# Performance work log

Measured on AMD Instinct MI355X. Metric: run time of the kernel, lower is better.

Reference implementation:

```python
import math
import jax, jax.numpy as jnp
import numpy as np

CHUNK = 32
EPS = 1e-5


def l2norm(x):
    return x * jax.lax.rsqrt(jnp.sum(x * x, -1, keepdims=True))


def causal_dwconv(x, w):
    # x: (B, C, L); w: (C, K) depthwise causal conv (left pad K-1)
    C, K = w.shape
    return jax.lax.conv_general_dilated(x, w[:, None, :], (1,), [(K - 1, 0)], feature_group_count=C)


def per_head_stats(x):
    # x: (B,L,H,D) -> (B,L,H,4): mean, var(pop), abs-mean, l2-norm
    mean = jnp.mean(x, -1, keepdims=True)
    var = jnp.mean(x * x, -1, keepdims=True) - mean * mean
    abs_mean = jnp.mean(jnp.abs(x), -1, keepdims=True)
    l2 = jnp.sqrt(jnp.sum(x * x, -1, keepdims=True))
    return jnp.concatenate([mean, var, abs_mean, l2], -1)


def delta_rule_chunkwise(q, k, v, beta, chunk=CHUNK):
    # q,k: (B,H,L,dk); v: (B,H,L,dv); beta: (B,H,L)
    b, h, L, dk = q.shape
    dv = v.shape[-1]
    pad = (-L) % chunk
    if pad:
        pc = ((0, 0), (0, 0), (0, pad), (0, 0))
        q, k, v = (jnp.pad(t, pc) for t in (q, k, v))
        beta = jnp.pad(beta, ((0, 0), (0, 0), (0, pad)))
    Lp = L + pad
    n = Lp // chunk
    q = l2norm(q)
    k = l2norm(k)
    v = v * beta[..., None]
    kb = k * beta[..., None]
    resh = lambda t: t.reshape(b, h, n, chunk, t.shape[-1])
    q, k, v, kb = map(resh, (q, k, v, kb))
    tri = jnp.triu(jnp.ones((chunk, chunk), bool))          # incl. diag
    strict = jnp.triu(jnp.ones((chunk, chunk), bool), 1)    # above diag
    A = jnp.where(tri, 0.0, -jnp.einsum('bhncd,bhned->bhnce', kb, k))
    # forward-substitution inverse of (I - strict_lower) as in the torch loop
    for i in range(1, chunk):
        upd = jnp.einsum('...k,...kj->...j', A[..., i, :], A[..., :, :i])
        A = A.at[..., i, :i].add(upd)
    inv = A + jnp.eye(chunk, dtype=A.dtype)
    u = inv @ v   # (b,h,n,c,dv)
    w = inv @ kb  # (b,h,n,c,dk)

    def step(S, xs):
        qi, ki, ui, wi = xs  # (b,h,c,d)
        attn = jnp.where(strict, 0.0, qi @ jnp.swapaxes(ki, -1, -2))
        u_adj = ui - wi @ S
        out_i = qi @ S + attn @ u_adj
        S = S + jnp.swapaxes(ki, -1, -2) @ u_adj
        return S, out_i

    xs = tuple(jnp.moveaxis(t, 2, 0) for t in (q, k, u, w))
    S0 = jnp.zeros((b, h, dk, dv), q.dtype)
    S, outs = jax.lax.scan(step, S0, xs)
    out = jnp.moveaxis(outs, 0, 2).reshape(b, h, Lp, dv)[:, :, :L]
    return out, S


def reference(hidden_states, q_proj_w, k_proj_w, v_proj_w, b_proj_w,
              q_conv_w, k_conv_w, v_conv_w, fir_short_w, fir_long_w,
              fuse_w1, fuse_b1, fuse_w2, fuse_b2, logit_temp,
              res_scale_short, res_scale_long, o_norm_w, o_proj_w):
    B, L, D = hidden_states.shape
    H = fir_short_w.shape[0]

    def shortconv(x, w):  # x: (B,L,C)
        y = causal_dwconv(jnp.swapaxes(x, 1, 2), w)
        return jax.nn.silu(jnp.swapaxes(y, 1, 2))

    q = shortconv(hidden_states @ q_proj_w.T, q_conv_w)
    k = shortconv(hidden_states @ k_proj_w.T, k_conv_w)
    v = shortconv(hidden_states @ v_proj_w.T, v_conv_w)
    q = q.reshape(B, L, H, -1)
    k = k.reshape(B, L, H, -1)
    v_direct = v.reshape(B, L, H, -1)
    beta = jax.nn.sigmoid(hidden_states @ b_proj_w.T)  # (B,L,H)

    delta_out, _S = delta_rule_chunkwise(
        jnp.transpose(q, (0, 2, 1, 3)), jnp.transpose(k, (0, 2, 1, 3)),
        jnp.transpose(v_direct, (0, 2, 1, 3)), jnp.transpose(beta, (0, 2, 1)))
    delta_out = jnp.transpose(delta_out, (0, 2, 1, 3))

    def fir(x, filt):  # x: (B,L,H,Dh); filt: (H,Dh,K)
        hh, dd, kk = filt.shape
        xf = jnp.swapaxes(x.reshape(B, L, hh * dd), 1, 2)
        y = causal_dwconv(xf, filt.reshape(hh * dd, kk))
        return jnp.swapaxes(y, 1, 2).reshape(B, L, hh, dd)

    local_short = fir(v_direct, fir_short_w)
    local_long = fir(v_direct, fir_long_w)

    stats = jnp.concatenate([per_head_stats(t) for t in
                             (local_short, local_long, delta_out, v_direct)], -1)  # (B,L,H,16)
    hs_exp = jnp.broadcast_to(hidden_states[:, :, None, :], (B, L, H, D))
    gate_in = jnp.concatenate([hs_exp, stats], -1)
    hdn = jax.nn.gelu(gate_in @ fuse_w1.T + fuse_b1, approximate=False)
    logits = hdn @ fuse_w2.T + fuse_b2  # (B,L,H,4)
    temp = jax.nn.softplus(logit_temp) + 1e-4
    fw = jax.nn.softmax(logits / temp, -1)

    o = (fw[..., 0:1] * local_short + fw[..., 1:2] * local_long
         + fw[..., 2:3] * delta_out + fw[..., 3:4] * v_direct)
    o = o + res_scale_short * local_short + res_scale_long * local_long
    o = o * jax.lax.rsqrt(jnp.mean(o * o, -1, keepdims=True) + EPS) * o_norm_w
    return o.reshape(B, L, -1) @ o_proj_w.T


def setup_inputs() -> dict:
    key = jax.random.key(0)
    ks = jax.random.split(key, 16)
    B, L, D, H = 2, 4096, 1024, 4
    dk, dv = D, D
    dh = dv // H
    gate_in_dim = D + 16
    gate_hidden = D * 2 // 2
    s = 0.02
    f32 = jnp.float32
    return {
        'hidden_states': jax.random.normal(ks[0], (B, L, D), f32),
        'q_proj_w': jax.random.normal(ks[1], (dk, D), f32) * s,
        'k_proj_w': jax.random.normal(ks[2], (dk, D), f32) * s,
        'v_proj_w': jax.random.normal(ks[3], (dv, D), f32) * s,
        'b_proj_w': jax.random.normal(ks[4], (H, D), f32) * s,
        'q_conv_w': jax.random.normal(ks[5], (dk, 4), f32) * 0.1,
        'k_conv_w': jax.random.normal(ks[6], (dk, 4), f32) * 0.1,
        'v_conv_w': jax.random.normal(ks[7], (dv, 4), f32) * 0.1,
        'fir_short_w': jax.random.normal(ks[8], (H, dh, 5), f32) * 0.02,
        'fir_long_w': jax.random.normal(ks[9], (H, dh, 64), f32) * 0.02,
        'fuse_w1': jax.random.normal(ks[10], (gate_hidden, gate_in_dim), f32) * s,
        'fuse_b1': jnp.zeros((gate_hidden,), f32),
        'fuse_w2': jax.random.normal(ks[11], (4, gate_hidden), f32) * s,
        'fuse_b2': jnp.array([-1.0, -1.0, 1.0, 3.0], f32),
        'logit_temp': jnp.full((1,), math.log(math.expm1(0.7)), f32),
        'res_scale_short': jnp.full((1,), 0.1, f32),
        'res_scale_long': jnp.full((1,), 0.1, f32),
        'o_norm_w': jnp.ones((dh,), f32),
        'o_proj_w': jax.random.normal(ks[12], (D, dv), f32) * s,
    }
```

## Files before the change

### kernel.cpp

```cpp
#include <hip/hip_runtime.h>
#include <hip/hip_bf16.h>

#define BB 2
#define LL 4096
#define DD 1024
#define HH 4
#define DH 256
#define CH 32
#define NC (LL/CH)
#define BL (BB*LL)
#define BLD ((size_t)BB*LL*DD)

typedef __attribute__((ext_vector_type(8))) short short8;
typedef __attribute__((ext_vector_type(4))) float floatx4;

__device__ __forceinline__ float bf2f(unsigned short u) {
    union { float f; unsigned int i; } x; x.i = ((unsigned int)u) << 16; return x.f;
}
__device__ __forceinline__ float bflo(unsigned int u) {
    union { float f; unsigned int i; } x; x.i = u << 16; return x.f;
}
__device__ __forceinline__ float bfhi(unsigned int u) {
    union { float f; unsigned int i; } x; x.i = u & 0xFFFF0000u; return x.f;
}
__device__ __forceinline__ unsigned short f2bf(float f) {
    union { float f; unsigned int i; } x; x.f = f;
    unsigned int r = x.i + 0x7FFFu + ((x.i >> 16) & 1u);
    return (unsigned short)(r >> 16);
}
__device__ __forceinline__ unsigned int pkbf(float a, float b) {
    unsigned int ua = __float_as_uint(a) + 0x8000u;
    unsigned int ub = __float_as_uint(b) + 0x8000u;
    return __builtin_amdgcn_perm(ub, ua, 0x07060302);
}
__device__ __forceinline__ void lds_barrier() {
    __builtin_amdgcn_s_waitcnt(0xC07F);
    __builtin_amdgcn_s_barrier();
}

typedef __attribute__((address_space(1))) const unsigned int as1_uint;
typedef __attribute__((address_space(3))) unsigned int as3_uint;
__device__ __forceinline__ void dma16(const void* g, void* l) {
    __builtin_amdgcn_global_load_lds((as1_uint*)g, (as3_uint*)l, 16, 0, 0);
}

__global__ __launch_bounds__(256) void cvt_bf_k(
    const float* __restrict__ x, unsigned short* __restrict__ y)
{
    size_t i = ((size_t)blockIdx.x * 256 + threadIdx.x) * 4;
    float4 v = *(const float4*)(x + i);
    ushort4 o;
    o.x = f2bf(v.x); o.y = f2bf(v.y); o.z = f2bf(v.z); o.w = f2bf(v.w);
    *(ushort4*)(y + i) = o;
}

__global__ __launch_bounds__(256) void w1s_prep_k(
    const float* __restrict__ w1, unsigned short* __restrict__ w1s)
{
    int idx = blockIdx.x * 256 + threadIdx.x;
    int e = idx >> 4, s = idx & 15;
    w1s[idx] = f2bf(w1[(size_t)e * 1040 + 1024 + s]);
}

__global__ __launch_bounds__(256) void gemm_mfma(
    const float* __restrict__ A, int lda,
    const float* __restrict__ W, int ldw,
    const float* __restrict__ bias,
    float* __restrict__ C, int ldc, int K)
{
    __shared__ unsigned short Abuf[128][56];
    __shared__ unsigned short Bbuf[128][56];
    const int t = threadIdx.x;
    const int wave = t >> 6, lane = t & 63;
    const int wm = wave >> 1, wn = wave & 1;
    const int row0 = blockIdx.y * 128, col0 = blockIdx.x * 128;

    floatx4 acc[4][4];
#pragma unroll
    for (int i = 0; i < 4; ++i)
#pragma unroll
        for (int j = 0; j < 4; ++j) acc[i][j] = (floatx4){0.f, 0.f, 0.f, 0.f};

    const int fr = lane & 15, fk = (lane >> 4) * 8;

    for (int kt = 0; kt < K; kt += 32) {
        __syncthreads();
#pragma unroll
        for (int it = 0; it < 2; ++it) {
            int idx = t + it * 256;
            int r = idx >> 2, s = (idx & 3) * 8;
            const float* ap = A + (size_t)(row0 + r) * lda + kt + s;
            float4 a0 = *(const float4*)(ap);
            float4 a1 = *(const float4*)(ap + 4);
            ushort4 p0, p1;
            p0.x = f2bf(a0.x); p0.y = f2bf(a0.y); p0.z = f2bf(a0.z); p0.w = f2bf(a0.w);
            p1.x = f2bf(a1.x); p1.y = f2bf(a1.y); p1.z = f2bf(a1.z); p1.w = f2bf(a1.w);
            *(ushort4*)&Abuf[r][s]     = p0;
            *(ushort4*)&Abuf[r][s + 4] = p1;
            const float* wp = W + (size_t)(col0 + r) * ldw + kt + s;
            float4 b0 = *(const float4*)(wp);
            float4 b1 = *(const float4*)(wp + 4);
            ushort4 q0, q1;
            q0.x = f2bf(b0.x); q0.y = f2bf(b0.y); q0.z = f2bf(b0.z); q0.w = f2bf(b0.w);
            q1.x = f2bf(b1.x); q1.y = f2bf(b1.y); q1.z = f2bf(b1.z); q1.w = f2bf(b1.w);
            *(ushort4*)&Bbuf[r][s]     = q0;
            *(ushort4*)&Bbuf[r][s + 4] = q1;
        }
        __syncthreads();

        short8 afrag[4], bfrag[4];
#pragma unroll
        for (int i = 0; i < 4; ++i) {
            afrag[i] = *(const short8*)&Abuf[wm * 64 + i * 16 + fr][fk];
            bfrag[i] = *(const short8*)&Bbuf[wn * 64 + i * 16 + fr][fk];
        }
#pragma unroll
        for (int i = 0; i < 4; ++i)
#pragma unroll
            for (int j = 0; j < 4; ++j)
                acc[i][j] = __builtin_amdgcn_mfma_f32_16x16x32_bf16(
                    afrag[i], bfrag[j], acc[i][j], 0, 0, 0);
    }

    const int fc = lane & 15, frow = (lane >> 4) * 4;
#pragma unroll
    for (int j = 0; j < 4; ++j) {
        int col = col0 + wn * 64 + j * 16 + fc;
        float bv = bias ? bias[col] : 0.0f;
#pragma unroll
        for (int i = 0; i < 4; ++i) {
#pragma unroll
            for (int r = 0; r < 4; ++r) {
                int row = row0 + wm * 64 + i * 16 + frow + r;
                C[(size_t)row * ldc + col] = acc[i][j][r] + bv;
            }
        }
    }
}

__global__ __launch_bounds__(256) void gemm_bb(
    const unsigned short* __restrict__ A, int lda,
    const unsigned short* __restrict__ B, int ldb,
    float* __restrict__ C, int ldc, int K)
{
    __shared__ unsigned short Abuf[128][56];
    __shared__ unsigned short Bbuf[128][56];
    const int t = threadIdx.x;
    const int wave = t >> 6, lane = t & 63;
    const int wm = wave >> 1, wn = wave & 1;
    const int row0 = blockIdx.y * 128, col0 = blockIdx.x * 128;

    floatx4 acc[4][4];
#pragma unroll
    for (int i = 0; i < 4; ++i)
#pragma unroll
        for (int j = 0; j < 4; ++j) acc[i][j] = (floatx4){0.f, 0.f, 0.f, 0.f};

    const int fr = lane & 15, fk = (lane >> 4) * 8;

    for (int kt = 0; kt < K; kt += 32) {
        __syncthreads();
#pragma unroll
        for (int it = 0; it < 2; ++it) {
            int idx = t + it * 256;
            int r = idx >> 2, s = (idx & 3) * 8;
            uint4 av = *(const uint4*)(A + (size_t)(row0 + r) * lda + kt + s);
            *(uint4*)&Abuf[r][s] = av;
            uint4 bv = *(const uint4*)(B + (size_t)(col0 + r) * ldb + kt + s);
            *(uint4*)&Bbuf[r][s] = bv;
        }
        __syncthreads();

        short8 afrag[4], bfrag[4];
#pragma unroll
        for (int i = 0; i < 4; ++i) {
            afrag[i] = *(const short8*)&Abuf[wm * 64 + i * 16 + fr][fk];
            bfrag[i] = *(const short8*)&Bbuf[wn * 64 + i * 16 + fr][fk];
        }
#pragma unroll
        for (int i = 0; i < 4; ++i)
#pragma unroll
            for (int j = 0; j < 4; ++j)
                acc[i][j] = __builtin_amdgcn_mfma_f32_16x16x32_bf16(
                    afrag[i], bfrag[j], acc[i][j], 0, 0, 0);
    }

    const int fc = lane & 15, frow = (lane >> 4) * 4;
#pragma unroll
    for (int j = 0; j < 4; ++j) {
        int col = col0 + wn * 64 + j * 16 + fc;
#pragma unroll
        for (int i = 0; i < 4; ++i) {
#pragma unroll
            for (int r = 0; r < 4; ++r) {
                int row = row0 + wm * 64 + i * 16 + frow + r;
                C[(size_t)row * ldc + col] = acc[i][j][r];
            }
        }
    }
}

__global__ __launch_bounds__(256) void convnorm_qk_k(
    const float* __restrict__ x, const float* __restrict__ w,
    unsigned short* __restrict__ y)
{
    int bl = blockIdx.x >> 2;
    int h  = blockIdx.x & 3;
    int l  = bl & (LL - 1);
    int d  = threadIdx.x;
    int c  = h * DH + d;
    const float* wp = w + (size_t)c * 4;
    const float* xp = x + (size_t)bl * DD + c;
    float acc = wp[3] * xp[0];
    if (l >= 1) acc += wp[2] * xp[-(int)DD];
    if (l >= 2) acc += wp[1] * xp[-2*(int)DD];
    if (l >= 3) acc += wp[0] * xp[-3*(int)DD];
    acc = acc / (1.0f + expf(-acc));
    float s = acc * acc;
#pragma unroll
    for (int off = 32; off > 0; off >>= 1) s += __shfl_down(s, off);
    __shared__ float red[4];
    int wv = threadIdx.x >> 6, ln = threadIdx.x & 63;
    if (ln == 0) red[wv] = s;
    __syncthreads();
    float tot = red[0] + red[1] + red[2] + red[3];
    y[(size_t)bl * DD + c] = f2bf(acc * rsqrtf(tot));
}

__global__ __launch_bounds__(256) void conv_silu_k(
    const float* __restrict__ x, const float* __restrict__ w, float* __restrict__ y)
{
    size_t idx = (size_t)blockIdx.x * 256 + threadIdx.x;
    int c = (int)(idx & (DD - 1));
    int bl = (int)(idx >> 10);
    int l = bl & (LL - 1);
    const float* wp = w + (size_t)c * 4;
    const float* xp = x + (size_t)bl * DD + c;
    float acc = wp[3] * xp[0];
    if (l >= 1) acc += wp[2] * xp[-(int)DD];
    if (l >= 2) acc += wp[1] * xp[-2*(int)DD];
    if (l >= 3) acc += wp[0] * xp[-3*(int)DD];
    y[idx] = acc / (1.0f + expf(-acc));
}

template<int K>
__global__ __launch_bounds__(256) void fir2_k(
    const float* __restrict__ x, const float* __restrict__ filt, float* __restrict__ y)
{
    const int ctile = blockIdx.x & 15;
    const int ltile = (blockIdx.x >> 4) & 63;
    const int b = blockIdx.x >> 10;
    const int RT = 64 + K - 1;
    __shared__ float xs[RT][64];
    __shared__ float fs[64][K + 1];
    const int t = threadIdx.x;
    const int l0 = ltile * 64;

    for (int i = t; i < RT * 16; i += 256) {
        int li = i >> 4, c4 = (i & 15) * 4;
        int l = l0 - (K - 1) + li;
        float4 v = make_float4(0.f, 0.f, 0.f, 0.f);
        if (l >= 0)
            v = *(const float4*)(x + ((size_t)b * LL + l) * DD + ctile * 64 + c4);
        *(float4*)&xs[li][c4] = v;
    }
    for (int i = t; i < 64 * K; i += 256) {
        fs[i / K][i % K] = filt[(size_t)ctile * 64 * K + i];
    }
    __syncthreads();

    const int c = t & 63, lg = t >> 6;
    float acc[16];
#pragma unroll
    for (int o = 0; o < 16; ++o) acc[o] = 0.f;
#pragma unroll
    for (int j = 0; j < 16 + K - 1; ++j) {
        float xv = xs[lg * 16 + j][c];
#pragma unroll
        for (int o = 0; o < 16; ++o) {
            int tap = j - o;
            if (tap >= 0 && tap < K) acc[o] += fs[c][tap] * xv;
        }
    }
    size_t base = ((size_t)b * LL + l0 + lg * 16) * DD + ctile * 64 + c;
#pragma unroll
    for (int o = 0; o < 16; ++o)
        y[base + (size_t)o * DD] = acc[o];
}

__global__ __launch_bounds__(256) void beta_k(
    const float* __restrict__ hs, const float* __restrict__ bw, float* __restrict__ beta)
{
    int bl = blockIdx.x;
    const float* xr = hs + (size_t)bl * DD;
    float a0=0.f,a1=0.f,a2=0.f,a3=0.f;
    for (int k = threadIdx.x; k < DD; k += 256) {
        float xv = xr[k];
        a0 += xv * bw[k];
        a1 += xv * bw[DD + k];
        a2 += xv * bw[2*DD + k];
        a3 += xv * bw[3*DD + k];
    }
#pragma unroll
    for (int off = 32; off > 0; off >>= 1) {
        a0 += __shfl_down(a0, off); a1 += __shfl_down(a1, off);
        a2 += __shfl_down(a2, off); a3 += __shfl_down(a3, off);
    }
    __shared__ float red[4][4];
    int wv = threadIdx.x >> 6, ln = threadIdx.x & 63;
    if (ln == 0) { red[wv][0]=a0; red[wv][1]=a1; red[wv][2]=a2; red[wv][3]=a3; }
    __syncthreads();
    if (threadIdx.x < 4) {
        int h = threadIdx.x;
        float s = red[0][h] + red[1][h] + red[2][h] + red[3][h];
        beta[(size_t)bl * HH + h] = 1.0f / (1.0f + expf(-s));
    }
}

__global__ __launch_bounds__(256) void tr_k(
    const unsigned short* __restrict__ k, unsigned short* __restrict__ kT)
{
    int et = blockIdx.x & 3;
    int lt = (blockIdx.x >> 2) & 63;
    int bh = blockIdx.x >> 8;
    int h = bh & 3, b = bh >> 2;
    __shared__ unsigned short tile[64][72];
    int t = threadIdx.x;
    int tr = t >> 4;
    int tc = (t & 15) * 4;
#pragma unroll
    for (int i = 0; i < 4; ++i) {
        int l = tr + i * 16;
        ushort4 v = *(const ushort4*)(k + ((size_t)b * LL + lt*64 + l) * DD + h * DH + et*64 + tc);
        *(ushort4*)&tile[l][tc] = v;
    }
    __syncthreads();
#pragma unroll
    for (int i = 0; i < 4; ++i) {
        int e = tr + i * 16;
        ushort4 v;
        v.x = tile[tc+0][e]; v.y = tile[tc+1][e];
        v.z = tile[tc+2][e]; v.w = tile[tc+3][e];
        *(ushort4*)(kT + ((size_t)bh * DH + et*64 + e) * LL + (size_t)lt*64 + tc) = v;
    }
}

__global__ __launch_bounds__(256) void tru_k(
    const unsigned short* __restrict__ u, unsigned short* __restrict__ uT)
{
    int et = blockIdx.x & 3;
    int lt = (blockIdx.x >> 2) & 63;
    int bh = blockIdx.x >> 8;
    __shared__ unsigned short tile[64][72];
    int t = threadIdx.x;
    int tr = t >> 4;
    int tc = (t & 15) * 4;
#pragma unroll
    for (int i = 0; i < 4; ++i) {
        int l = tr + i * 16;
        ushort4 v = *(const ushort4*)(u + ((size_t)bh * LL + lt*64 + l) * DH + et*64 + tc);
        *(ushort4*)&tile[l][tc] = v;
    }
    __syncthreads();
#pragma unroll
    for (int i = 0; i < 4; ++i) {
        int e = tr + i * 16;
        ushort4 v;
        v.x = tile[tc+0][e]; v.y = tile[tc+1][e];
        v.z = tile[tc+2][e]; v.w = tile[tc+3][e];
        *(ushort4*)(uT + ((size_t)bh * DH + et*64 + e) * LL + (size_t)lt*64 + tc) = v;
    }
}

__global__ __launch_bounds__(256) void chunk_prep_k(
    const unsigned short* __restrict__ q, const unsigned short* __restrict__ k,
    const float* __restrict__ v, const float* __restrict__ beta,
    unsigned short* __restrict__ u_out, unsigned short* __restrict__ w_out,
    unsigned short* __restrict__ attn_out)
{
    int ci = blockIdx.x & (NC - 1);
    int bh = blockIdx.x >> 7;
    int h = bh & (HH - 1), b = bh >> 2;
    __shared__ float kt[CH][DH + 4];
    __shared__ float Am[CH][CH + 1];
    __shared__ float Ab[CH][CH + 1];
    __shared__ float bet[CH];
    int t = threadIdx.x;
    size_t qgbase = (size_t)b * LL + (size_t)ci * CH;

    for (int i = t; i < CH * (DH / 4); i += 256) {
        int r = i >> 6;
        int c4 = (i & 63) * 4;
        ushort4 kv = *(const ushort4*)(k + (qgbase + r) * DD + h * DH + c4);
        kt[r][c4+0] = bf2f(kv.x); kt[r][c4+1] = bf2f(kv.y);
        kt[r][c4+2] = bf2f(kv.z); kt[r][c4+3] = bf2f(kv.w);
    }
    if (t < CH) bet[t] = beta[(qgbase + t) * HH + h];
    __syncthreads();

    int c = t >> 3, e0 = (t & 7) * 4;
    {
        float accA[4] = {0,0,0,0}, accT[4] = {0,0,0,0};
        const unsigned short* qrow = q + (qgbase + c) * DD + h * DH;
        for (int d0 = 0; d0 < DH; d0 += 4) {
            float4 kc = *(const float4*)&kt[c][d0];
            ushort4 qv = *(const ushort4*)(qrow + d0);
            float qx = bf2f(qv.x), qy = bf2f(qv.y), qz = bf2f(qv.z), qw = bf2f(qv.w);
#pragma unroll
            for (int e = 0; e < 4; ++e) {
                float4 ke = *(const float4*)&kt[e0 + e][d0];
                accA[e] += kc.x*ke.x + kc.y*ke.y + kc.z*ke.z + kc.w*ke.w;
                accT[e] += qx*ke.x + qy*ke.y + qz*ke.z + qw*ke.w;
            }
        }
        float bc = bet[c];
        size_t abase = (size_t)blockIdx.x * (CH * CH) + (size_t)c * CH;
#pragma unroll
        for (int e = 0; e < 4; ++e) {
            int ee = e0 + e;
            Am[c][ee] = (ee < c) ? (-bc * accA[e]) : 0.0f;
            attn_out[abase + ee] = (ee <= c) ? f2bf(accT[e]) : (unsigned short)0;
        }
    }
    __syncthreads();

    for (int i = 1; i < CH; ++i) {
        float upd = 0.0f;
        if (t < i) {
#pragma unroll
            for (int kk = 0; kk < CH; ++kk) upd += Am[i][kk] * Am[kk][t];
        }
        __syncthreads();
        if (t < i) Am[i][t] += upd;
        __syncthreads();
    }

    for (int i = t; i < CH * CH; i += 256) {
        int cc = i >> 5, ee = i & 31;
        float val = Am[cc][ee] + (cc == ee ? 1.0f : 0.0f);
        Ab[cc][ee] = val * bet[ee];
    }
    __syncthreads();

    int c2 = t >> 3, dd0 = (t & 7) * 32;
    float accu[32];
#pragma unroll
    for (int j = 0; j < 32; ++j) accu[j] = 0.0f;
    for (int e = 0; e < CH; ++e) {
        float ab = Ab[c2][e];
        const float* vrow = v + (qgbase + e) * DD + h * DH + dd0;
#pragma unroll
        for (int j4 = 0; j4 < 8; ++j4) {
            float4 v4 = *(const float4*)(vrow + j4 * 4);
            accu[j4*4+0] += ab * v4.x; accu[j4*4+1] += ab * v4.y;
            accu[j4*4+2] += ab * v4.z; accu[j4*4+3] += ab * v4.w;
        }
    }
    size_t obase = ((size_t)bh * LL + (size_t)ci * CH + c2) * DH + dd0;
#pragma unroll
    for (int j4 = 0; j4 < 8; ++j4) {
        ushort4 o;
        o.x = f2bf(accu[j4*4+0]); o.y = f2bf(accu[j4*4+1]);
        o.z = f2bf(accu[j4*4+2]); o.w = f2bf(accu[j4*4+3]);
        *(ushort4*)(u_out + obase + j4*4) = o;
    }

#pragma unroll
    for (int j = 0; j < 32; ++j) accu[j] = 0.0f;
    for (int e = 0; e < CH; ++e) {
        float ab = Ab[c2][e];
#pragma unroll
        for (int j4 = 0; j4 < 8; ++j4) {
            float4 v4 = *(const float4*)&kt[e][dd0 + j4*4];
            accu[j4*4+0] += ab * v4.x; accu[j4*4+1] += ab * v4.y;
            accu[j4*4+2] += ab * v4.z; accu[j4*4+3] += ab * v4.w;
        }
    }
#pragma unroll
    for (int j4 = 0; j4 < 8; ++j4) {
        ushort4 o;
        o.x = f2bf(accu[j4*4+0]); o.y = f2bf(accu[j4*4+1]);
        o.z = f2bf(accu[j4*4+2]); o.w = f2bf(accu[j4*4+3]);
        *(ushort4*)(w_out + obase + j4*4) = o;
    }
}

__global__ __launch_bounds__(256, 1) void scan10_k(
    const unsigned short* __restrict__ q, const unsigned short* __restrict__ kT,
    const unsigned short* __restrict__ uT, const unsigned short* __restrict__ w,
    const unsigned short* __restrict__ attn, float* __restrict__ dout)
{
    const int bh = blockIdx.x & 7;
    const int jb = blockIdx.x >> 3;
    const int h = bh & (HH - 1), b = bh >> 2;
    const int jcol = jb * 16;
    const int wave = threadIdx.x >> 6, lane = threadIdx.x & 63;
    const int lr = lane & 15, lg = lane >> 4;
    const int half = wave & 1;
    const bool isQ = wave >= 2;

    #define OW 0
    #define OQ 16384
    #define OK2 32768
    #define OA 49152
    #define OU 51200
    __shared__ char slotmem[2][52224];
    __shared__ unsigned short SbT[2][16][264];
    __shared__ unsigned short uadjT[2][16][40];

    floatx4 Sacc[4];
#pragma unroll
    for (int mt = 0; mt < 4; ++mt) Sacc[mt] = (floatx4){0.f,0.f,0.f,0.f};

    const char* wbB  = (const char*)(w  + (size_t)bh * LL * DH);
    const char* qbB  = (const char*)(q  + (size_t)b * LL * DD + h * DH);
    const char* kbB  = (const char*)(kT + (size_t)bh * DH * LL);
    const char* uTbB = (const char*)(uT + (size_t)bh * DH * LL);
    const char* atB  = (const char*)(attn + (size_t)bh * NC * (CH * CH));
    float* db = dout + (size_t)bh * LL * DH;

    const int lane16 = lane * 16;
    int pw[4], pq[4], pkt[4];
#pragma unroll
    for (int j = 0; j < 4; ++j) {
        int i = wave + 4 * j;
        int L = i * 1024 + lane16;
        { int row = L >> 9, g = (L >> 4) & 31, gs = g ^ (row & 7);
          pw[j] = row * 512 + gs * 16; }
        { int row = L >> 9, g = (L >> 4) & 31, gs = g ^ (row & 7);
          pq[j] = row * 2048 + gs * 16; }
        { int row = L >> 6, g = (L >> 4) & 3, gs = g ^ (row & 3);
          pkt[j] = row * 8192 + gs * 16; }
    }
    int pat = 0, put = 0;
    if (wave < 2) { int L = wave * 1024 + lane16;
        int row = L >> 6, g = (L >> 4) & 3, gs = g ^ (row & 3);
        pat = row * 64 + gs * 16; }
    else if (wave == 2) { int L = lane16;
        int row = L >> 6, g = (L >> 4) & 3;
        put = (jcol + row) * 8192 + g * 16; }

    const int row_o = half * 16 + lr;
    int opo[8];
#pragma unroll
    for (int kt = 0; kt < 8; ++kt)
        opo[kt] = row_o * 512 + (((kt * 4 + lg) ^ (row_o & 7)) * 16);
    int opk[4];
#pragma unroll
    for (int mt = 0; mt < 4; ++mt) {
        int rk = 64 * wave + 16 * mt + lr;
        opk[mt] = rk * 64 + ((lg ^ (rk & 3)) * 16);
    }
    const int opa = row_o * 64 + ((lg ^ (row_o & 3)) * 16);
    const int opu = lr * 64 + half * 32 + lg * 8;

    {
        char* sb = &slotmem[0][0];
#pragma unroll
        for (int j = 0; j < 4; ++j) {
            int i = wave + 4 * j;
            dma16(wbB + pw[j],  sb + OW  + i * 1024);
            dma16(qbB + pq[j],  sb + OQ  + i * 1024);
            dma16(kbB + pkt[j], sb + OK2 + i * 1024);
        }
        if (wave < 2)       dma16(atB + pat,  sb + OA + wave * 1024);
        else if (wave == 2) dma16(uTbB + put, sb + OU);
    }

#pragma unroll 2
    for (int ci = 0; ci < NC; ++ci) {
        const int p = ci & 1;
        const int l0 = ci * CH;

#pragma unroll
        for (int mt = 0; mt < 4; ++mt) {
            int e0 = 64 * wave + 16 * mt + lg * 4;
            *(unsigned int*)&SbT[p][lr][e0]     = pkbf(Sacc[mt][0], Sacc[mt][1]);
            *(unsigned int*)&SbT[p][lr][e0 + 2] = pkbf(Sacc[mt][2], Sacc[mt][3]);
        }

        asm volatile("s_waitcnt vmcnt(0)" ::: "memory");
        lds_barrier();

        {
            const int cn = (ci + 1 < NC) ? (ci + 1) : ci;
            const size_t lnW = (size_t)(cn * CH) * 512;
            const size_t lnQ = (size_t)(cn * CH) * 2048;
            const size_t lnK = (size_t)(cn * CH) * 2;
            char* sb = &slotmem[p ^ 1][0];
#pragma unroll
            for (int j = 0; j < 4; ++j) {
                int i = wave + 4 * j;
                dma16(wbB + lnW + pw[j],  sb + OW  + i * 1024);
                dma16(qbB + lnQ + pq[j],  sb + OQ  + i * 1024);
                dma16(kbB + lnK + pkt[j], sb + OK2 + i * 1024);
            }
            if (wave < 2)       dma16(atB + (size_t)cn * 2048 + pat, sb + OA + wave * 1024);
            else if (wave == 2) dma16(uTbB + lnK + put, sb + OU);
        }

        const char* sp = &slotmem[p][0];
        const char* ab = sp + (isQ ? OQ : OW);

        floatx4 Pa = (floatx4){0.f,0.f,0.f,0.f}, Pb = Pa;
#pragma unroll
        for (int kt = 0; kt < 4; ++kt) {
            short8 s0 = *(const short8*)&SbT[p][lr][(2*kt)   * 32 + lg * 8];
            short8 s1 = *(const short8*)&SbT[p][lr][(2*kt+1) * 32 + lg * 8];
            short8 a0 = *(const short8*)(ab + opo[2*kt]);
            short8 a1 = *(const short8*)(ab + opo[2*kt+1]);
            Pa = __builtin_amdgcn_mfma_f32_16x16x32_bf16(a0, s0, Pa, 0,0,0);
            Pb = __builtin_amdgcn_mfma_f32_16x16x32_bf16(a1, s1, Pb, 0,0,0);
        }
        floatx4 P = Pa + Pb;

        if (!isQ) {
            ushort4 u4 = *(const ushort4*)(sp + OU + opu);
            float ua0 = bf2f(u4.x) - P[0];
            float ua1 = bf2f(u4.y) - P[1];
            float ua2 = bf2f(u4.z) - P[2];
            float ua3 = bf2f(u4.w) - P[3];
            int cc0 = half * 16 + lg * 4;
            *(unsigned int*)&uadjT[p][lr][cc0]     = pkbf(ua0, ua1);
            *(unsigned int*)&uadjT[p][lr][cc0 + 2] = pkbf(ua2, ua3);
        }
        lds_barrier();

        short8 ub = *(const short8*)&uadjT[p][lr][lg * 8];

        if (isQ) {
            short8 paR = *(const short8*)(sp + OA + opa);
            floatx4 Ot = __builtin_amdgcn_mfma_f32_16x16x32_bf16(paR, ub, P, 0,0,0);
#pragma unroll
            for (int r = 0; r < 4; ++r)
                db[(size_t)(l0 + half * 16 + lg * 4 + r) * DH + jcol + lr] = Ot[r];
        }

#pragma unroll
        for (int mt = 0; mt < 4; ++mt) {
            short8 pkR = *(const short8*)(sp + OK2 + opk[mt]);
            Sacc[mt] = __builtin_amdgcn_mfma_f32_16x16x32_bf16(pkR, ub, Sacc[mt], 0,0,0);
        }
    }
    #undef OW
    #undef OQ
    #undef OK2
    #undef OA
    #undef OU
}

__global__ __launch_bounds__(256) void stats_k(
    const float* __restrict__ ls, const float* __restrict__ llb,
    const float* __restrict__ dox, const float* __restrict__ v,
    float* __restrict__ stats)
{
    int bl = blockIdx.x;
    int b = bl >> 12, l = bl & (LL - 1);
    int wv = threadIdx.x >> 6, ln = threadIdx.x & 63;
    size_t ibase = (size_t)bl * DD + wv * DH;
    size_t dbase = (((size_t)(b * HH + wv)) * LL + l) * DH;
#pragma unroll
    for (int tn = 0; tn < 4; ++tn) {
        const float* p; size_t base;
        if (tn == 0)      { p = ls;  base = ibase; }
        else if (tn == 1) { p = llb; base = ibase; }
        else if (tn == 2) { p = dox; base = dbase; }
        else              { p = v;   base = ibase; }
        float4 x = *(const float4*)(p + base + ln * 4);
        float sm = x.x + x.y + x.z + x.w;
        float sq = x.x*x.x + x.y*x.y + x.z*x.z + x.w*x.w;
        float sa = fabsf(x.x) + fabsf(x.y) + fabsf(x.z) + fabsf(x.w);
#pragma unroll
        for (int off = 32; off > 0; off >>= 1) {
            sm += __shfl_down(sm, off);
            sq += __shfl_down(sq, off);
            sa += __shfl_down(sa, off);
        }
        if (ln == 0) {
            float mean = sm * (1.0f / DH);
            float var = sq * (1.0f / DH) - mean * mean;
            float am = sa * (1.0f / DH);
            float l2 = sqrtf(sq);
            *(float4*)(stats + (size_t)bl * 64 + wv * 16 + tn * 4) =
                make_float4(mean, var, am, l2);
        }
    }
}

__global__ __launch_bounds__(256) void gate_fin2_k(
    const float* __restrict__ hpart, const float* __restrict__ stats,
    const unsigned short* __restrict__ w1s,
    const float* __restrict__ w2, const float* __restrict__ b2,
    const float* __restrict__ ltemp, float* __restrict__ fw)
{
    const int bl = blockIdx.x;
    const int t = threadIdx.x;
    const float temp = log1pf(expf(ltemp[0])) + 1e-4f;
    __shared__ float st[HH][16];
    __shared__ float red[4][16];
    __shared__ float fin[16];
    if (t < 64) st[t >> 4][t & 15] = stats[(size_t)bl * 64 + t];

    const int e0 = t * 4;
    float4 hp4 = *(const float4*)(hpart + (size_t)bl * DD + e0);
    float hp[4] = {hp4.x, hp4.y, hp4.z, hp4.w};
    float w2a[4][4];
#pragma unroll
    for (int j = 0; j < 4; ++j) {
        float4 wv = *(const float4*)(w2 + (size_t)j * 1024 + e0);
        w2a[j][0] = wv.x; w2a[j][1] = wv.y; w2a[j][2] = wv.z; w2a[j][3] = wv.w;
    }
    uint4 wpk[8];
    const uint4* wp = (const uint4*)(w1s + (size_t)e0 * 16);
#pragma unroll
    for (int i = 0; i < 8; ++i) wpk[i] = wp[i];
    __syncthreads();

    float lg[4][4];
#pragma unroll
    for (int h = 0; h < 4; ++h)
#pragma unroll
        for (int j = 0; j < 4; ++j) lg[h][j] = 0.0f;

#pragma unroll
    for (int ii = 0; ii < 4; ++ii) {
        float xh[4] = {hp[ii], hp[ii], hp[ii], hp[ii]};
        unsigned arr[8] = {wpk[ii*2].x, wpk[ii*2].y, wpk[ii*2].z, wpk[ii*2].w,
                           wpk[ii*2+1].x, wpk[ii*2+1].y, wpk[ii*2+1].z, wpk[ii*2+1].w};
#pragma unroll
        for (int p = 0; p < 8; ++p) {
            float wlo = bflo(arr[p]), whi = bfhi(arr[p]);
            int s = p * 2;
#pragma unroll
            for (int h = 0; h < 4; ++h)
                xh[h] += st[h][s] * wlo + st[h][s + 1] * whi;
        }
#pragma unroll
        for (int h = 0; h < 4; ++h) {
            float x = xh[h];
            float gct = 0.5f * x * (1.0f + erff(x * 0.70710678118654752f));
            lg[h][0] += gct * w2a[0][ii];
            lg[h][1] += gct * w2a[1][ii];
            lg[h][2] += gct * w2a[2][ii];
            lg[h][3] += gct * w2a[3][ii];
        }
    }

#pragma unroll
    for (int h = 0; h < 4; ++h)
#pragma unroll
        for (int j = 0; j < 4; ++j)
#pragma unroll
            for (int off = 32; off > 0; off >>= 1)
                lg[h][j] += __shfl_down(lg[h][j], off);

    const int wv = t >> 6, ln = t & 63;
    if (ln == 0) {
#pragma unroll
        for (int h = 0; h < 4; ++h)
#pragma unroll
            for (int j = 0; j < 4; ++j) red[wv][h * 4 + j] = lg[h][j];
    }
    __syncthreads();
    if (t < 16) {
        float s = red[0][t] + red[1][t] + red[2][t] + red[3][t] + b2[t & 3];
        fin[t] = s / temp;
    }
    __syncthreads();
    if (t < 4) {
        float l0 = fin[t*4], l1 = fin[t*4+1], l2 = fin[t*4+2], l3 = fin[t*4+3];
        float m = fmaxf(fmaxf(l0, l1), fmaxf(l2, l3));
        float e0x = expf(l0-m), e1 = expf(l1-m), e2 = expf(l2-m), e3 = expf(l3-m);
        float inv = 1.0f / (e0x + e1 + e2 + e3);
        *(float4*)(fw + (size_t)bl * 16 + t * 4) = make_float4(e0x*inv, e1*inv, e2*inv, e3*inv);
    }
}

__global__ __launch_bounds__(256) void combine_k(
    const float* __restrict__ ls, const float* __restrict__ llb,
    const float* __restrict__ dox, const float* __restrict__ v,
    const float* __restrict__ fw, const float* __restrict__ rss,
    const float* __restrict__ rsl, const float* __restrict__ onw,
    float* __restrict__ opre)
{
    int h = blockIdx.x & (HH - 1);
    int bl = blockIdx.x >> 2;
    int b = bl >> 12, l = bl & (LL - 1);
    int d = threadIdx.x;
    size_t i1 = (size_t)blockIdx.x * DH + d;
    size_t i2 = (((size_t)(b * HH + h)) * LL + l) * DH + d;
    const float* fwp = fw + (size_t)blockIdx.x * 4;
    float f0 = fwp[0], f1 = fwp[1], f2 = fwp[2], f3 = fwp[3];
    float aS = rss[0], aL = rsl[0];
    float vls = ls[i1], vll = llb[i1], vd = dox[i2], vv = v[i1];
    float o = f0*vls + f1*vll + f2*vd + f3*vv + aS*vls + aL*vll;
    float s = o * o;
#pragma unroll
    for (int off = 32; off > 0; off >>= 1) s += __shfl_down(s, off);
    __shared__ float red[4];
    int wv = threadIdx.x >> 6, ln = threadIdx.x & 63;
    if (ln == 0) red[wv] = s;
    __syncthreads();
    float ms = (red[0] + red[1] + red[2] + red[3]) * (1.0f / DH);
    opre[(size_t)bl * DD + h * DH + d] = o * rsqrtf(ms + 1e-5f) * onw[d];
}

extern "C" void kernel_launch(void* const* d_in, const int* in_sizes, int n_in,
                              void* d_out, int out_size, void* d_ws, size_t ws_size,
                              hipStream_t stream)
{
    const float* hs  = (const float*)d_in[0];
    const float* qw  = (const float*)d_in[1];
    const float* kw  = (const float*)d_in[2];
    const float* vw  = (const float*)d_in[3];
    const float* bw  = (const float*)d_in[4];
    const float* qcw = (const float*)d_in[5];
    const float* kcw = (const float*)d_in[6];
    const float* vcw = (const float*)d_in[7];
    const float* fsw = (const float*)d_in[8];
    const float* flw = (const float*)d_in[9];
    const float* w1  = (const float*)d_in[10];
    const float* b1  = (const float*)d_in[11];
    const float* w2  = (const float*)d_in[12];
    const float* b2  = (const float*)d_in[13];
    const float* lt  = (const float*)d_in[14];
    const float* rss = (const float*)d_in[15];
    const float* rsl = (const float*)d_in[16];
    const float* onw = (const float*)d_in[17];
    const float* opw = (const float*)d_in[18];
    float* out = (float*)d_out;

    float* wsf = (float*)d_ws;
    float* tmp   = wsf;
    unsigned short* ktbuf = (unsigned short*)tmp;
    unsigned short* uTbuf = (unsigned short*)(wsf + BLD/2);
    float* vbuf  = wsf + BLD;
    float* dbuf  = wsf + 2*BLD;
    unsigned short* hsb = (unsigned short*)(wsf + 2*BLD);
    unsigned short* qwb = (unsigned short*)(wsf + 2*BLD + BLD/2);
    unsigned short* kwb = qwb + (size_t)DD*DD;
    unsigned short* vwb = kwb + (size_t)DD*DD;
    unsigned short* qbuf = (unsigned short*)(wsf + 3*BLD);
    unsigned short* kbuf = qbuf + BLD;
    float* hpart = wsf + 3*BLD;
    float* opre  = wsf + 3*BLD;
    unsigned short* ubuf = (unsigned short*)(wsf + 4*BLD);
    unsigned short* wbuf = ubuf + BLD;
    float* llbuf = wsf + 4*BLD;
    float* lsbuf = tmp;
    unsigned short* attnb = (unsigned short*)(wsf + 5*BLD);
    float* statsb = wsf + 5*BLD + 524288;
    float* fwbuf  = statsb + (size_t)BL*HH*16;
    float* betab  = fwbuf + (size_t)BL*HH*4;
    unsigned short* w1sp = (unsigned short*)(betab + (size_t)BL*HH);

    dim3 gg(8, 64);

    cvt_bf_k<<<(int)(BLD/1024), 256, 0, stream>>>(hs, hsb);
    cvt_bf_k<<<1024, 256, 0, stream>>>(qw, qwb);
    cvt_bf_k<<<1024, 256, 0, stream>>>(kw, kwb);
    cvt_bf_k<<<1024, 256, 0, stream>>>(vw, vwb);
    w1s_prep_k<<<64, 256, 0, stream>>>(w1, w1sp);

    gemm_bb<<<gg, 256, 0, stream>>>(hsb, DD, qwb, DD, tmp, DD, DD);
    convnorm_qk_k<<<BL*HH, 256, 0, stream>>>(tmp, qcw, qbuf);
    gemm_bb<<<gg, 256, 0, stream>>>(hsb, DD, kwb, DD, tmp, DD, DD);
    convnorm_qk_k<<<BL*HH, 256, 0, stream>>>(tmp, kcw, kbuf);
    gemm_bb<<<gg, 256, 0, stream>>>(hsb, DD, vwb, DD, tmp, DD, DD);
    conv_silu_k<<<(int)(BLD/256), 256, 0, stream>>>(tmp, vcw, vbuf);

    beta_k<<<BL, 256, 0, stream>>>(hs, bw, betab);

    tr_k<<<8*64*4, 256, 0, stream>>>(kbuf, ktbuf);
    chunk_prep_k<<<BB*HH*NC, 256, 0, stream>>>(qbuf, kbuf, vbuf, betab, ubuf, wbuf, attnb);
    tru_k<<<8*64*4, 256, 0, stream>>>(ubuf, uTbuf);

    scan10_k<<<BB*HH*16, 256, 0, stream>>>(qbuf, ktbuf, uTbuf, wbuf, attnb, dbuf);

    fir2_k<5><<<BB*64*16, 256, 0, stream>>>(vbuf, fsw, lsbuf);
    fir2_k<64><<<BB*64*16, 256, 0, stream>>>(vbuf, flw, llbuf);

    stats_k<<<BL, 256, 0, stream>>>(lsbuf, llbuf, dbuf, vbuf, statsb);

    gemm_mfma<<<gg, 256, 0, stream>>>(hs, DD, w1, 1040, b1, hpart, DD, DD);
    gate_fin2_k<<<BL, 256, 0, stream>>>(hpart, statsb, w1sp, w2, b2, lt, fwbuf);

    combine_k<<<BL*HH, 256, 0, stream>>>(lsbuf, llbuf, dbuf, vbuf, fwbuf, rss, rsl, onw, opre);

    gemm_mfma<<<gg, 256, 0, stream>>>(opre, DD, opw, DD, nullptr, out, DD, DD);
}
```

Before: 990.5 us.

## Rewrite chunk prep with MFMA, wave-shuffle inverse, and fused u transpose

Replaces the scalar-FMA chunk preparation kernel with one that computes the k·k and q·k Gram matrices via bf16 MFMA. The triangular inverse now runs in a single wave using shuffles instead of 62 block-wide barriers. The u and w products use MFMA with a hi/lo bf16 split of the inverse to keep precision. The kernel writes u directly in transposed layout, which removes the separate transpose kernel and its extra global round trip. The cost is bf16 rounding of v inside the MFMA and scattered 2-byte writes for w.

```diff
diff --git a/kernel.cpp b/kernel.cpp
--- a/kernel.cpp
+++ b/kernel.cpp
@@ -345,143 +345,130 @@
     }
 }
 
-__global__ __launch_bounds__(256) void tru_k(
-    const unsigned short* __restrict__ u, unsigned short* __restrict__ uT)
-{
-    int et = blockIdx.x & 3;
-    int lt = (blockIdx.x >> 2) & 63;
-    int bh = blockIdx.x >> 8;
-    __shared__ unsigned short tile[64][72];
-    int t = threadIdx.x;
-    int tr = t >> 4;
-    int tc = (t & 15) * 4;
-#pragma unroll
-    for (int i = 0; i < 4; ++i) {
-        int l = tr + i * 16;
-        ushort4 v = *(const ushort4*)(u + ((size_t)bh * LL + lt*64 + l) * DH + et*64 + tc);
-        *(ushort4*)&tile[l][tc] = v;
-    }
-    __syncthreads();
-#pragma unroll
-    for (int i = 0; i < 4; ++i) {
-        int e = tr + i * 16;
-        ushort4 v;
-        v.x = tile[tc+0][e]; v.y = tile[tc+1][e];
-        v.z = tile[tc+2][e]; v.w = tile[tc+3][e];
-        *(ushort4*)(uT + ((size_t)bh * DH + et*64 + e) * LL + (size_t)lt*64 + tc) = v;
-    }
-}
-
-__global__ __launch_bounds__(256) void chunk_prep_k(
+__global__ __launch_bounds__(256) void chunk_prep2_k(
     const unsigned short* __restrict__ q, const unsigned short* __restrict__ k,
-    const float* __restrict__ v, const float* __restrict__ beta,
-    unsigned short* __restrict__ u_out, unsigned short* __restrict__ w_out,
+    const unsigned short* __restrict__ kT, const float* __restrict__ v,
+    const float* __restrict__ beta,
+    unsigned short* __restrict__ uT, unsigned short* __restrict__ w_out,
     unsigned short* __restrict__ attn_out)
 {
-    int ci = blockIdx.x & (NC - 1);
-    int bh = blockIdx.x >> 7;
-    int h = bh & (HH - 1), b = bh >> 2;
-    __shared__ float kt[CH][DH + 4];
-    __shared__ float Am[CH][CH + 1];
-    __shared__ float Ab[CH][CH + 1];
-    __shared__ float bet[CH];
-    int t = threadIdx.x;
-    size_t qgbase = (size_t)b * LL + (size_t)ci * CH;
-
-    for (int i = t; i < CH * (DH / 4); i += 256) {
-        int r = i >> 6;
-        int c4 = (i & 63) * 4;
-        ushort4 kv = *(const ushort4*)(k + (qgbase + r) * DD + h * DH + c4);
-        kt[r][c4+0] = bf2f(kv.x); kt[r][c4+1] = bf2f(kv.y);
-        kt[r][c4+2] = bf2f(kv.z); kt[r][c4+3] = bf2f(kv.w);
-    }
-    if (t < CH) bet[t] = beta[(qgbase + t) * HH + h];
-    __syncthreads();
-
-    int c = t >> 3, e0 = (t & 7) * 4;
+    const int ci = blockIdx.x & (NC - 1);
+    const int bh = blockIdx.x >> 7;
+    const int h = bh & (HH - 1), b = bh >> 2;
+    __shared__ unsigned short kL[32][264];
+    __shared__ unsigned short qL[32][264];
+    __shared__ float vL[32][260];
+    __shared__ float AmL[32][33];
+    __shared__ unsigned short AbH[32][40];
+    __shared__ unsigned short AbL2[32][40];
+    __shared__ float betL[32];
+    const int t = threadIdx.x;
+    const int wave = t >> 6, lane = t & 63;
+    const int lr = lane & 15, lg = lane >> 4;
+    const int l0 = ci * CH;
+    const size_t rowbase = (size_t)b * LL + l0;
+
+    for (int i = t; i < 1024; i += 256) {
+        int r = i >> 5, s8 = (i & 31) * 8;
+        *(uint4*)&kL[r][s8] = *(const uint4*)(k + (rowbase + r) * DD + h * DH + s8);
+        *(uint4*)&qL[r][s8] = *(const uint4*)(q + (rowbase + r) * DD + h * DH + s8);
+    }
+    for (int i = t; i < 2048; i += 256) {
+        int e = i >> 6, d4 = (i & 63) * 4;
+        *(float4*)&vL[e][d4] = *(const float4*)(v + (rowbase + e) * DD + h * DH + d4);
+    }
+    if (t < 32) betL[t] = beta[(rowbase + t) * HH + h];
+    __syncthreads();
+
+    const int mt = wave >> 1, nt = wave & 1;
+    floatx4 accA = (floatx4){0.f,0.f,0.f,0.f}, accT = accA;
+#pragma unroll
+    for (int ks = 0; ks < 8; ++ks) {
+        short8 bk = *(const short8*)&kL[nt * 16 + lr][ks * 32 + lg * 8];
+        short8 ak = *(const short8*)&kL[mt * 16 + lr][ks * 32 + lg * 8];
+        short8 aq = *(const short8*)&qL[mt * 16 + lr][ks * 32 + lg * 8];
+        accA = __builtin_amdgcn_mfma_f32_16x16x32_bf16(ak, bk, accA, 0, 0, 0);
+        accT = __builtin_amdgcn_mfma_f32_16x16x32_bf16(aq, bk, accT, 0, 0, 0);
+    }
     {
-        float accA[4] = {0,0,0,0}, accT[4] = {0,0,0,0};
-        const unsigned short* qrow = q + (qgbase + c) * DD + h * DH;
-        for (int d0 = 0; d0 < DH; d0 += 4) {
-            float4 kc = *(const float4*)&kt[c][d0];
-            ushort4 qv = *(const ushort4*)(qrow + d0);
-            float qx = bf2f(qv.x), qy = bf2f(qv.y), qz = bf2f(qv.z), qw = bf2f(qv.w);
-#pragma unroll
-            for (int e = 0; e < 4; ++e) {
-                float4 ke = *(const float4*)&kt[e0 + e][d0];
-                accA[e] += kc.x*ke.x + kc.y*ke.y + kc.z*ke.z + kc.w*ke.w;
-                accT[e] += qx*ke.x + qy*ke.y + qz*ke.z + qw*ke.w;
+        const size_t abase = (size_t)blockIdx.x * (CH * CH);
+        const int ee = nt * 16 + lr;
+#pragma unroll
+        for (int r = 0; r < 4; ++r) {
+            int c = mt * 16 + lg * 4 + r;
+            float bc = betL[c];
+            AmL[c][ee] = (ee < c) ? (-bc * accA[r]) : 0.0f;
+            attn_out[abase + (size_t)c * CH + ee] =
+                (ee <= c) ? f2bf(accT[r]) : (unsigned short)0;
+        }
+    }
+    __syncthreads();
+
+    const unsigned short* kTg = kT + (size_t)bh * DH * LL;
+    short8 wB[4];
+#pragma unroll
+    for (int n = 0; n < 4; ++n)
+        wB[n] = *(const short8*)(kTg + (size_t)(wave * 64 + n * 16 + lr) * LL + l0 + lg * 8);
+
+    if (wave == 0) {
+        const int j = lane & 31;
+        float col[32];
+#pragma unroll
+        for (int c = 0; c < 32; ++c) col[c] = AmL[c][j];
+#pragma unroll
+        for (int i = 1; i < 32; ++i) {
+            float u0 = 0.f, u1 = 0.f;
+#pragma unroll
+            for (int kk = 0; kk < 32; kk += 2) {
+                if (kk < i)     u0 += __shfl(col[i], kk) * col[kk];
+                if (kk + 1 < i) u1 += __shfl(col[i], kk + 1) * col[kk + 1];
             }
-        }
-        float bc = bet[c];
-        size_t abase = (size_t)blockIdx.x * (CH * CH) + (size_t)c * CH;
-#pragma unroll
-        for (int e = 0; e < 4; ++e) {
-            int ee = e0 + e;
-            Am[c][ee] = (ee < c) ? (-bc * accA[e]) : 0.0f;
-            attn_out[abase + ee] = (ee <= c) ? f2bf(accT[e]) : (unsigned short)0;
-        }
-    }
-    __syncthreads();
-
-    for (int i = 1; i < CH; ++i) {
-        float upd = 0.0f;
-        if (t < i) {
-#pragma unroll
-            for (int kk = 0; kk < CH; ++kk) upd += Am[i][kk] * Am[kk][t];
-        }
-        __syncthreads();
-        if (t < i) Am[i][t] += upd;
-        __syncthreads();
-    }
-
-    for (int i = t; i < CH * CH; i += 256) {
-        int cc = i >> 5, ee = i & 31;
-        float val = Am[cc][ee] + (cc == ee ? 1.0f : 0.0f);
-        Ab[cc][ee] = val * bet[ee];
-    }
-    __syncthreads();
-
-    int c2 = t >> 3, dd0 = (t & 7) * 32;
-    float accu[32];
-#pragma unroll
-    for (int j = 0; j < 32; ++j) accu[j] = 0.0f;
-    for (int e = 0; e < CH; ++e) {
-        float ab = Ab[c2][e];
-        const float* vrow = v + (qgbase + e) * DD + h * DH + dd0;
-#pragma unroll
-        for (int j4 = 0; j4 < 8; ++j4) {
-            float4 v4 = *(const float4*)(vrow + j4 * 4);
-            accu[j4*4+0] += ab * v4.x; accu[j4*4+1] += ab * v4.y;
-            accu[j4*4+2] += ab * v4.z; accu[j4*4+3] += ab * v4.w;
-        }
-    }
-    size_t obase = ((size_t)bh * LL + (size_t)ci * CH + c2) * DH + dd0;
-#pragma unroll
-    for (int j4 = 0; j4 < 8; ++j4) {
-        ushort4 o;
-        o.x = f2bf(accu[j4*4+0]); o.y = f2bf(accu[j4*4+1]);
-        o.z = f2bf(accu[j4*4+2]); o.w = f2bf(accu[j4*4+3]);
-        *(ushort4*)(u_out + obase + j4*4) = o;
-    }
-
-#pragma unroll
-    for (int j = 0; j < 32; ++j) accu[j] = 0.0f;
-    for (int e = 0; e < CH; ++e) {
-        float ab = Ab[c2][e];
-#pragma unroll
-        for (int j4 = 0; j4 < 8; ++j4) {
-            float4 v4 = *(const float4*)&kt[e][dd0 + j4*4];
-            accu[j4*4+0] += ab * v4.x; accu[j4*4+1] += ab * v4.y;
-            accu[j4*4+2] += ab * v4.z; accu[j4*4+3] += ab * v4.w;
-        }
-    }
-#pragma unroll
-    for (int j4 = 0; j4 < 8; ++j4) {
-        ushort4 o;
-        o.x = f2bf(accu[j4*4+0]); o.y = f2bf(accu[j4*4+1]);
-        o.z = f2bf(accu[j4*4+2]); o.w = f2bf(accu[j4*4+3]);
-        *(ushort4*)(w_out + obase + j4*4) = o;
+            if (j < i) col[i] += u0 + u1;
+        }
+        if (lane < 32) {
+            const float bj = betL[j];
+#pragma unroll
+            for (int c = 0; c < 32; ++c) {
+                float val = (col[c] + (c == j ? 1.0f : 0.0f)) * bj;
+                unsigned short hi = f2bf(val);
+                AbH[c][j] = hi;
+                AbL2[c][j] = f2bf(val - bf2f(hi));
+            }
+        }
+    }
+    __syncthreads();
+
+    short8 AH[2], ALo[2];
+#pragma unroll
+    for (int m = 0; m < 2; ++m) {
+        AH[m]  = *(const short8*)&AbH[m * 16 + lr][lg * 8];
+        ALo[m] = *(const short8*)&AbL2[m * 16 + lr][lg * 8];
+    }
+    const size_t uTbase = (size_t)bh * DH * LL;
+    const size_t wbase  = (size_t)bh * LL * DH;
+#pragma unroll
+    for (int n = 0; n < 4; ++n) {
+        const int d = wave * 64 + n * 16 + lr;
+        union { short8 s8; unsigned int u[4]; } vf;
+#pragma unroll
+        for (int p2 = 0; p2 < 4; ++p2)
+            vf.u[p2] = pkbf(vL[lg * 8 + p2 * 2][d], vL[lg * 8 + p2 * 2 + 1][d]);
+#pragma unroll
+        for (int m = 0; m < 2; ++m) {
+            floatx4 au = (floatx4){0.f,0.f,0.f,0.f};
+            au = __builtin_amdgcn_mfma_f32_16x16x32_bf16(AH[m],  vf.s8, au, 0, 0, 0);
+            au = __builtin_amdgcn_mfma_f32_16x16x32_bf16(ALo[m], vf.s8, au, 0, 0, 0);
+            ushort4 ou;
+            ou.x = f2bf(au[0]); ou.y = f2bf(au[1]); ou.z = f2bf(au[2]); ou.w = f2bf(au[3]);
+            *(ushort4*)(uT + uTbase + (size_t)d * LL + l0 + m * 16 + lg * 4) = ou;
+
+            floatx4 aw = (floatx4){0.f,0.f,0.f,0.f};
+            aw = __builtin_amdgcn_mfma_f32_16x16x32_bf16(AH[m],  wB[n], aw, 0, 0, 0);
+            aw = __builtin_amdgcn_mfma_f32_16x16x32_bf16(ALo[m], wB[n], aw, 0, 0, 0);
+#pragma unroll
+            for (int r = 0; r < 4; ++r)
+                w_out[wbase + (size_t)(l0 + m * 16 + lg * 4 + r) * DH + d] = f2bf(aw[r]);
+        }
     }
 }
 
@@ -872,8 +859,8 @@
     beta_k<<<BL, 256, 0, stream>>>(hs, bw, betab);
 
     tr_k<<<8*64*4, 256, 0, stream>>>(kbuf, ktbuf);
-    chunk_prep_k<<<BB*HH*NC, 256, 0, stream>>>(qbuf, kbuf, vbuf, betab, ubuf, wbuf, attnb);
-    tru_k<<<8*64*4, 256, 0, stream>>>(ubuf, uTbuf);
+    chunk_prep2_k<<<BB*HH*NC, 256, 0, stream>>>(qbuf, kbuf, ktbuf, vbuf, betab,
+                                                uTbuf, wbuf, attnb);
 
     scan10_k<<<BB*HH*16, 256, 0, stream>>>(qbuf, ktbuf, uTbuf, wbuf, attnb, dbuf);
 
```

Measured after the change: 876.4 us. 11.5% less time.
